# Kernel optimization log

Hardware: AMD Instinct MI355X
Metric: run time of the kernel (lower is better)

Reference implementation:

```python
import jax, jax.numpy as jnp
import numpy as np

B, T, E, H, D = 4, 2048, 1024, 16, 64  # batch, seq(block_size), n_embed, num_heads, hidden_dim


def setup_inputs() -> dict:
    key = jax.random.key(0)
    ks = jax.random.split(key, 10)
    s_in = 1.0 / np.sqrt(E)
    return {
        "x": jax.random.normal(ks[0], (B, T, E), dtype=jnp.float32),
        "Wq": jax.random.normal(ks[1], (H, E, D), dtype=jnp.float32) * s_in,
        "bq": jnp.zeros((H, D), dtype=jnp.float32),
        "Wk": jax.random.normal(ks[2], (H, E, D), dtype=jnp.float32) * s_in,
        "bk": jnp.zeros((H, D), dtype=jnp.float32),
        "Wv": jax.random.normal(ks[3], (H, E, D), dtype=jnp.float32) * s_in,
        "bv": jnp.zeros((H, D), dtype=jnp.float32),
        "Wp": jax.random.normal(ks[4], (E, E), dtype=jnp.float32) * s_in,
        "bp": jnp.zeros((E,), dtype=jnp.float32),
    }


def reference(x, Wq, bq, Wk, bk, Wv, bv, Wp, bp):
    # Batched equivalent of the per-head Python loop: each head h computes
    # causal scaled-dot-product attention with its own Q/K/V projections.
    q = jnp.einsum("bte,hed->bhtd", x, Wq) + bq[None, :, None, :]
    k = jnp.einsum("bte,hed->bhtd", x, Wk) + bk[None, :, None, :]
    v = jnp.einsum("bte,hed->bhtd", x, Wv) + bv[None, :, None, :]
    scale = 1.0 / jnp.sqrt(jnp.asarray(D, dtype=x.dtype))
    scores = jnp.einsum("bhtd,bhsd->bhts", q, k) * scale  # [B,H,T,T]
    causal = jnp.tril(jnp.ones((T, T), dtype=bool))
    scores = jnp.where(causal[None, None, :, :], scores, jnp.asarray(-jnp.inf, dtype=x.dtype))
    att = jax.nn.softmax(scores, axis=-1)
    head_out = jnp.einsum("bhts,bhsd->bhtd", att, v)  # [B,H,T,D]
    # concat heads along last dim: [B,T,H*D] == [B,T,E]
    cat = head_out.transpose(0, 2, 1, 3).reshape(B, T, H * D)
    out = cat @ Wp + bp  # final projection (dropout is identity in eval)
    return out
```

## Files before the change

kernel.cpp:

```cpp
#include <hip/hip_runtime.h>


typedef __attribute__((ext_vector_type(8))) __bf16 bf16x8;
typedef __attribute__((ext_vector_type(4))) float f32x4;
typedef __attribute__((ext_vector_type(16))) float f32x16;
typedef __attribute__((ext_vector_type(4))) unsigned int u32x4;
typedef __attribute__((ext_vector_type(2))) unsigned int u32x2;
typedef unsigned short u16;
typedef unsigned int u32;

#define DEV __device__ __forceinline__

#define QK_SCALE 0.18033688011112042f

DEV u16 f2bf(float f) {
  u32 u = __builtin_bit_cast(u32, f);
  u += 0x7fffu + ((u >> 16) & 1u);
  return (u16)(u >> 16);
}
DEV u32 pack2(float a, float b) { return (u32)f2bf(a) | ((u32)f2bf(b) << 16); }

DEV float exp2_hw(float x) { float r; asm("v_exp_f32 %0, %1" : "=v"(r) : "v"(x)); return r; }
DEV u32 cvtpk_bf16(float lo, float hi) {
  u32 r; asm("v_cvt_pk_bf16_f32 %0, %1, %2" : "=v"(r) : "v"(lo), "v"(hi)); return r;
}
DEV void pl32swap(u32& a, u32& b) { asm("v_permlane32_swap_b32 %0, %1" : "+v"(a), "+v"(b)); }
DEV float max3f(float a, float b, float c) {
  float r; asm("v_max3_f32 %0, %1, %2, %3" : "=v"(r) : "v"(a), "v"(b), "v"(c)); return r;
}

DEV f32x16 zero16() { f32x16 z;
#pragma unroll
  for (int i = 0; i < 16; i++) z[i] = 0.f;
  return z; }

DEV void gll16(const u16* g, u16* l) {
  __builtin_amdgcn_global_load_lds((const __attribute__((address_space(1))) void*)g,
                                   (__attribute__((address_space(3))) void*)l, 16, 0, 0);
}

#define SCHEDB() __builtin_amdgcn_sched_barrier(0)
#define SBAR()   do { __builtin_amdgcn_s_barrier(); SCHEDB(); } while (0)
#define LGKM0()  do { asm volatile("s_waitcnt lgkmcnt(0)" ::: "memory"); SCHEDB(); } while (0)

__global__ __launch_bounds__(256) void prep_x_kernel(
    const float* __restrict__ x, const float* __restrict__ bq, const float* __restrict__ bk,
    const float* __restrict__ bv, u16* __restrict__ xbf, float* __restrict__ bqkv) {
  int gid = blockIdx.x * 256 + threadIdx.x;
  if (gid < 3072) {
    float v = (gid < 1024) ? bq[gid] * QK_SCALE : (gid < 2048 ? bk[gid - 1024] : bv[gid - 2048]);
    bqkv[gid] = v;
  }
  const float4* xv = (const float4*)x;
  float4 f0 = xv[(size_t)gid * 2];
  float4 f1 = xv[(size_t)gid * 2 + 1];
  u32x4 st;
  st.x = pack2(f0.x, f0.y); st.y = pack2(f0.z, f0.w);
  st.z = pack2(f1.x, f1.y); st.w = pack2(f1.z, f1.w);
  *(u32x4*)&xbf[(size_t)gid * 8] = st;
}

__global__ __launch_bounds__(256) void prep_w_kernel(
    const float* __restrict__ Wq, const float* __restrict__ Wk, const float* __restrict__ Wv,
    const float* __restrict__ Wp, u16* __restrict__ wqkvT, u16* __restrict__ wpT) {
  __shared__ float t[64][65];
  int bid = blockIdx.x, tid = threadIdx.x;
  int r0 = tid >> 6, c = tid & 63;
  if (bid < 768) {
    int p = bid >> 8, rem = bid & 255, h = rem >> 4, et = rem & 15;
    float sc = (p == 0) ? QK_SCALE : 1.0f;
    const float* src = (p == 0 ? Wq : (p == 1 ? Wk : Wv)) + ((size_t)h * 1024 + et * 64) * 64;
#pragma unroll
    for (int i = 0; i < 16; i++) { int e = r0 + i * 4; t[e][c] = src[(size_t)e * 64 + c]; }
    __syncthreads();
    u16* dst = wqkvT + ((size_t)p * 1024 + h * 64) * 1024 + et * 64;
#pragma unroll
    for (int i = 0; i < 16; i++) { int d = r0 + i * 4; dst[(size_t)d * 1024 + c] = f2bf(t[c][d] * sc); }
  } else {
    int b2 = bid - 768, rt = b2 >> 4, ct = b2 & 15;
#pragma unroll
    for (int i = 0; i < 16; i++) { int e = r0 + i * 4; t[e][c] = Wp[(size_t)(rt * 64 + e) * 1024 + ct * 64 + c]; }
    __syncthreads();
#pragma unroll
    for (int i = 0; i < 16; i++) { int f = r0 + i * 4; wpT[(size_t)(ct * 64 + f) * 1024 + rt * 64 + c] = f2bf(t[c][f]); }
  }
}

#define SLOT_U16 24576

DEV void stageA_unit(const u16* __restrict__ Asrc, int row0, int k0, int h, u16* An, int tid) {
#pragma unroll
  for (int jj = 0; jj < 2; jj++) {
    int idx = jj * 512 + tid;
    int row = h * 128 + (idx >> 3), slot = idx & 7;
    int ss = slot ^ (row & 7);
    gll16(Asrc + (size_t)(row0 + row) * 1024 + k0 + ss * 8, An + (size_t)row * 64 + slot * 8);
  }
}
DEV void stageB_unit(const u16* __restrict__ Bsrc, int row0, int k0, int h, u16* Bn, int tid) {
  int idx = tid;
  int row = h * 64 + (idx >> 3), slot = idx & 7;
  int ss = slot ^ (row & 7);
  gll16(Bsrc + (size_t)(row0 + row) * 1024 + k0 + ss * 8, Bn + (size_t)row * 64 + slot * 8);
}

DEV bf16x8 ldsAB(const u16* base, int row, int kk, int lg) {
  return *(const bf16x8*)&base[row * 64 + (((lg + kk * 4) ^ (row & 7)) * 8)];
}

__global__ __launch_bounds__(512, 2) void gemm256_kernel(
    const u16* __restrict__ A, const u16* __restrict__ Bt, const float* __restrict__ bias,
    int tilesN, int mode, u16* __restrict__ Qb, u16* __restrict__ Kb, u16* __restrict__ VTb,
    float* __restrict__ outF) {
  __shared__ u16 lds[3 * SLOT_U16];
  int nwg = gridDim.x;
  int bid = blockIdx.x;
  int swz = (bid % 8) * (nwg / 8) + bid / 8;
  int bm = swz / tilesN, bn = swz % tilesN;
  int tid = threadIdx.x;
  int lane = tid & 63, wave = tid >> 6;
  int wm = wave >> 1, wn = wave & 1;
  int lr = lane & 15, lg = lane >> 4;
  int aRow0 = bm * 256, bRow0 = bn * 128;
  int ar = wm * 64, br = wn * 64;

  f32x4 acc[4][4];
#pragma unroll
  for (int i = 0; i < 4; i++)
#pragma unroll
    for (int j = 0; j < 4; j++) acc[i][j] = f32x4{0.f, 0.f, 0.f, 0.f};

#pragma unroll
  for (int pt = 0; pt < 2; pt++) {
    u16* As = lds + pt * SLOT_U16;
    stageA_unit(A, aRow0, pt * 64, 0, As, tid);
    stageA_unit(A, aRow0, pt * 64, 1, As, tid);
    stageB_unit(Bt, bRow0, pt * 64, 0, As + 16384, tid);
    stageB_unit(Bt, bRow0, pt * 64, 1, As + 16384, tid);
  }
  asm volatile("s_waitcnt vmcnt(6)" ::: "memory");
  SCHEDB();
  SBAR();

  int rs = 0;
  for (int t = 0; t < 16; ++t) {
    u16* Ac = lds + rs * SLOT_U16;
    u16* Bc = Ac + 16384;
    int ws = rs + 2; if (ws >= 3) ws -= 3;
    u16* An = lds + ws * SLOT_U16;
    u16* Bn = An + 16384;
    int k2 = (t + 2) * 64;
    bool st = (t + 2) < 16;

    bf16x8 aLo[2][2], bLo[2][2];
#pragma unroll
    for (int i = 0; i < 2; i++)
#pragma unroll
      for (int kk = 0; kk < 2; kk++) aLo[i][kk] = ldsAB(Ac, ar + i * 16 + lr, kk, lg);
#pragma unroll
    for (int j = 0; j < 2; j++)
#pragma unroll
      for (int kk = 0; kk < 2; kk++) bLo[j][kk] = ldsAB(Bc, br + j * 16 + lr, kk, lg);
    if (st) stageA_unit(A, aRow0, k2, 0, An, tid);
    SBAR(); LGKM0();
    __builtin_amdgcn_s_setprio(1);
#pragma unroll
    for (int kk = 0; kk < 2; kk++)
#pragma unroll
      for (int i = 0; i < 2; i++)
#pragma unroll
        for (int j = 0; j < 2; j++)
          acc[i][j] = __builtin_amdgcn_mfma_f32_16x16x32_bf16(aLo[i][kk], bLo[j][kk], acc[i][j], 0, 0, 0);
    __builtin_amdgcn_s_setprio(0);
    SBAR();

    bf16x8 bHi[2][2];
#pragma unroll
    for (int j = 0; j < 2; j++)
#pragma unroll
      for (int kk = 0; kk < 2; kk++) bHi[j][kk] = ldsAB(Bc, br + 32 + j * 16 + lr, kk, lg);
    if (st) stageB_unit(Bt, bRow0, k2, 0, Bn, tid);
    SBAR(); LGKM0();
    __builtin_amdgcn_s_setprio(1);
#pragma unroll
    for (int kk = 0; kk < 2; kk++)
#pragma unroll
      for (int i = 0; i < 2; i++)
#pragma unroll
        for (int j = 0; j < 2; j++)
          acc[i][j + 2] = __builtin_amdgcn_mfma_f32_16x16x32_bf16(aLo[i][kk], bHi[j][kk], acc[i][j + 2], 0, 0, 0);
    __builtin_amdgcn_s_setprio(0);
    SBAR();

    bf16x8 aHi[2][2];
#pragma unroll
    for (int i = 0; i < 2; i++)
#pragma unroll
      for (int kk = 0; kk < 2; kk++) aHi[i][kk] = ldsAB(Ac, ar + 32 + i * 16 + lr, kk, lg);
    if (st) stageA_unit(A, aRow0, k2, 1, An, tid);
    SBAR(); LGKM0();
    __builtin_amdgcn_s_setprio(1);
#pragma unroll
    for (int kk = 0; kk < 2; kk++)
#pragma unroll
      for (int i = 0; i < 2; i++)
#pragma unroll
        for (int j = 0; j < 2; j++)
          acc[i + 2][j + 2] = __builtin_amdgcn_mfma_f32_16x16x32_bf16(aHi[i][kk], bHi[j][kk], acc[i + 2][j + 2], 0, 0, 0);
    __builtin_amdgcn_s_setprio(0);
    SBAR();

    if (st) stageB_unit(Bt, bRow0, k2, 1, Bn, tid);
    SBAR();
    __builtin_amdgcn_s_setprio(1);
#pragma unroll
    for (int kk = 0; kk < 2; kk++)
#pragma unroll
      for (int i = 0; i < 2; i++)
#pragma unroll
        for (int j = 0; j < 2; j++)
          acc[i + 2][j] = __builtin_amdgcn_mfma_f32_16x16x32_bf16(aHi[i][kk], bLo[j][kk], acc[i + 2][j], 0, 0, 0);
    __builtin_amdgcn_s_setprio(0);
    if (t < 14) { asm volatile("s_waitcnt vmcnt(6)" ::: "memory"); }
    else if (t == 14) { asm volatile("s_waitcnt vmcnt(0)" ::: "memory"); }
    SCHEDB();
    SBAR();

    rs = (rs == 2) ? 0 : rs + 1;
  }

  int crow = aRow0 + wm * 64;
  int ccol = bRow0 + wn * 64;
  if (mode == 0) {
#pragma unroll
    for (int j = 0; j < 4; j++) {
      int col = ccol + j * 16 + lr;
      float bb = bias[col];
      int p = col >> 10, h = (col >> 6) & 15, d = col & 63;
#pragma unroll
      for (int i = 0; i < 4; i++) {
        int row0 = crow + i * 16 + lg * 4;
        int b_ = row0 >> 11, t0 = row0 & 2047;
        if (p == 2) {
          u32x2 pv;
          pv.x = pack2(acc[i][j][0] + bb, acc[i][j][1] + bb);
          pv.y = pack2(acc[i][j][2] + bb, acc[i][j][3] + bb);
          *(u32x2*)&VTb[((size_t)(b_ * 16 + h) * 64 + d) * 2048 + t0] = pv;
        } else {
          u16* dst = (p == 0 ? Qb : Kb);
#pragma unroll
          for (int r = 0; r < 4; r++)
            dst[((size_t)(b_ * 16 + h) * 2048 + (t0 + r)) * 64 + d] = f2bf(acc[i][j][r] + bb);
        }
      }
    }
  } else {
#pragma unroll
    for (int j = 0; j < 4; j++) {
      int col = ccol + j * 16 + lr;
      float bb = bias[col];
#pragma unroll
      for (int i = 0; i < 4; i++) {
        int row0 = crow + i * 16 + lg * 4;
#pragma unroll
        for (int r = 0; r < 4; r++)
          outF[(size_t)(row0 + r) * 1024 + col] = acc[i][j][r] + bb;
      }
    }
  }
}

DEV void stage_kv128(const u16* __restrict__ Kh, const u16* __restrict__ Vh, int kv0,
                     u16* Ksb, u16* Vsb, int tid) {
#pragma unroll
  for (int j = 0; j < 4; j++) {
    int ci = j * 128 + tid;
    int row = ci >> 3, slot = ci & 7;
    int ss = slot ^ (row & 7);
    __builtin_amdgcn_global_load_lds(
        (const __attribute__((address_space(1))) void*)(Kh + (size_t)(kv0 + row) * 64 + ss * 8),
        (__attribute__((address_space(3))) void*)(Ksb + ci * 8), 16, 0, 0);
    __builtin_amdgcn_global_load_lds(
        (const __attribute__((address_space(1))) void*)(Vh + (size_t)row * 2048 + kv0 + ss * 8),
        (__attribute__((address_space(3))) void*)(Vsb + ci * 8), 16, 0, 0);
  }
}

__global__ __launch_bounds__(128, 2) void attn_kernel(
    const u16* __restrict__ Qb, const u16* __restrict__ Kb, const u16* __restrict__ VTb,
    u16* __restrict__ cat) {
  __shared__ u16 Ks[2][64 * 64];
  __shared__ u16 Vs[2][64 * 64];
  int bid = blockIdx.x;
  int t = 31 - (bid >> 6);
  int bh = bid & 63;
  int b = bh >> 4, h = bh & 15;
  int tid = threadIdx.x, wave = tid >> 6, lane = tid & 63;
  int l31 = lane & 31, hi = lane >> 5;
  int qrow = t * 64 + wave * 32 + l31;

  const u16* Qh = Qb + (size_t)bh * 2048 * 64;
  const u16* Kh = Kb + (size_t)bh * 2048 * 64;
  const u16* Vh = VTb + (size_t)bh * 64 * 2048;

  bf16x8 qf[4];
#pragma unroll
  for (int ks = 0; ks < 4; ks++)
    qf[ks] = *(const bf16x8*)&Qh[(size_t)qrow * 64 + ks * 16 + hi * 8];

  u32 loff[4];
#pragma unroll
  for (int ks = 0; ks < 4; ks++)
    loff[ks] = (u32)(l31 * 128 + (((ks * 2 + hi) ^ (l31 & 7)) * 16));

  f32x16 o0 = zero16(), o1 = zero16();
  float m_run = -1e30f, l_run = 0.f;
  int iters = t + 1;

  stage_kv128(Kh, Vh, 0, Ks[0], Vs[0], tid);
  __syncthreads();
  int cur = 0;

  for (int kvt = 0; kvt < iters; ++kvt) {
    int kv0 = kvt * 64;
    if (kvt + 1 < iters) stage_kv128(Kh, Vh, kv0 + 64, Ks[cur ^ 1], Vs[cur ^ 1], tid);

    f32x16 s0 = zero16(), s1 = zero16();
    const char* kb = (const char*)&Ks[cur][0];
    __builtin_amdgcn_s_setprio(1);
#pragma unroll
    for (int ks = 0; ks < 4; ks++) {
      bf16x8 k0 = *(const bf16x8*)(kb + loff[ks]);
      bf16x8 k1 = *(const bf16x8*)(kb + loff[ks] + 4096);
      s0 = __builtin_amdgcn_mfma_f32_32x32x16_bf16(k0, qf[ks], s0, 0, 0, 0);
      s1 = __builtin_amdgcn_mfma_f32_32x32x16_bf16(k1, qf[ks], s1, 0, 0, 0);
    }
    __builtin_amdgcn_s_setprio(0);

    if (kvt == t) {
      int relh = qrow - kv0 - 4 * hi;
#pragma unroll
      for (int r = 0; r < 16; r++) {
        int off = (r & 3) + 8 * (r >> 2);
        s0[r] = (off > relh) ? -1e30f : s0[r];
        s1[r] = (off + 32 > relh) ? -1e30f : s1[r];
      }
    }

    float ta = max3f(s0[0], s0[1], s0[2]);
    float tb = max3f(s0[4], s0[5], s0[6]);
    float tc = max3f(s0[8], s0[9], s0[10]);
    float td = max3f(s0[12], s0[13], s0[14]);
    ta = max3f(ta, s0[3], s1[0]);
    tb = max3f(tb, s0[7], s1[4]);
    tc = max3f(tc, s0[11], s1[8]);
    td = max3f(td, s0[15], s1[12]);
    ta = max3f(ta, s1[1], s1[2]);
    tb = max3f(tb, s1[5], s1[6]);
    tc = max3f(tc, s1[9], s1[10]);
    td = max3f(td, s1[13], s1[14]);
    ta = max3f(ta, s1[3], tb);
    tc = max3f(tc, s1[7], td);
    float tmax = max3f(ta, tc, s1[11]);
    tmax = fmaxf(tmax, s1[15]);
    tmax = fmaxf(tmax, __shfl_xor(tmax, 32));
    float corr = 1.f;
    if (!__all(tmax <= m_run + 8.f)) {
      float m_new = fmaxf(m_run, tmax);
      corr = exp2_hw(m_run - m_new);
      o0 = o0 * corr;
      o1 = o1 * corr;
      m_run = m_new;
    }
    float t0 = 0.f, t1 = 0.f, t2 = 0.f, t3 = 0.f;
#pragma unroll
    for (int j = 0; j < 4; j++) {
      float p00 = exp2_hw(s0[j * 4 + 0] - m_run); s0[j * 4 + 0] = p00; t0 += p00;
      float p01 = exp2_hw(s0[j * 4 + 1] - m_run); s0[j * 4 + 1] = p01; t1 += p01;
      float p02 = exp2_hw(s0[j * 4 + 2] - m_run); s0[j * 4 + 2] = p02; t2 += p02;
      float p03 = exp2_hw(s0[j * 4 + 3] - m_run); s0[j * 4 + 3] = p03; t3 += p03;
      float p10 = exp2_hw(s1[j * 4 + 0] - m_run); s1[j * 4 + 0] = p10; t0 += p10;
      float p11 = exp2_hw(s1[j * 4 + 1] - m_run); s1[j * 4 + 1] = p11; t1 += p11;
      float p12 = exp2_hw(s1[j * 4 + 2] - m_run); s1[j * 4 + 2] = p12; t2 += p12;
      float p13 = exp2_hw(s1[j * 4 + 3] - m_run); s1[j * 4 + 3] = p13; t3 += p13;
    }
    float ts = (t0 + t1) + (t2 + t3);
    ts += __shfl_xor(ts, 32);
    l_run = l_run * corr + ts;

    const char* vb = (const char*)&Vs[cur][0];
    __builtin_amdgcn_s_setprio(1);
#pragma unroll
    for (int ks = 0; ks < 4; ks++) {
      const f32x16& sb = (ks < 2) ? s0 : s1;
      int g2 = (ks & 1) * 8;
      u32 a  = cvtpk_bf16(sb[g2 + 0], sb[g2 + 1]);
      u32 c  = cvtpk_bf16(sb[g2 + 2], sb[g2 + 3]);
      u32 bb = cvtpk_bf16(sb[g2 + 4], sb[g2 + 5]);
      u32 d  = cvtpk_bf16(sb[g2 + 6], sb[g2 + 7]);
      pl32swap(a, bb);
      pl32swap(c, d);
      u32x4 wv; wv.x = a; wv.y = c; wv.z = bb; wv.w = d;
      bf16x8 pf = __builtin_bit_cast(bf16x8, wv);
      bf16x8 v0 = *(const bf16x8*)(vb + loff[ks]);
      bf16x8 v1 = *(const bf16x8*)(vb + loff[ks] + 4096);
      o0 = __builtin_amdgcn_mfma_f32_32x32x16_bf16(v0, pf, o0, 0, 0, 0);
      o1 = __builtin_amdgcn_mfma_f32_32x32x16_bf16(v1, pf, o1, 0, 0, 0);
    }
    __builtin_amdgcn_s_setprio(0);

    __syncthreads();
    cur ^= 1;
  }

  float li = 1.0f / l_run;
#pragma unroll
  for (int m = 0; m < 8; m++) {
    int dbase = 2 * (m & 1) + 8 * (m >> 1) + 4 * hi;
    u32 w0 = cvtpk_bf16(o0[2 * m] * li, o0[2 * m + 1] * li);
    u32 w1 = cvtpk_bf16(o1[2 * m] * li, o1[2 * m + 1] * li);
    *(u32*)&cat[(size_t)(b * 2048 + qrow) * 1024 + h * 64 + dbase] = w0;
    *(u32*)&cat[(size_t)(b * 2048 + qrow) * 1024 + h * 64 + 32 + dbase] = w1;
  }
}

extern "C" void kernel_launch(void* const* d_in, const int* in_sizes, int n_in,
                              void* d_out, int out_size, void* d_ws, size_t ws_size,
                              hipStream_t stream) {
  const float* x  = (const float*)d_in[0];
  const float* Wq = (const float*)d_in[1];
  const float* bq = (const float*)d_in[2];
  const float* Wk = (const float*)d_in[3];
  const float* bk = (const float*)d_in[4];
  const float* Wv = (const float*)d_in[5];
  const float* bv = (const float*)d_in[6];
  const float* Wp = (const float*)d_in[7];
  const float* bp = (const float*)d_in[8];

  char* w = (char*)d_ws;
  u16* xbf    = (u16*)w;                 w += (size_t)8192 * 1024 * 2;
  u16* wqkvT  = (u16*)w;                 w += (size_t)3072 * 1024 * 2;
  u16* wpT    = (u16*)w;                 w += (size_t)1024 * 1024 * 2;
  float* bqkv = (float*)w;               w += (size_t)3072 * 4;
  u16* Qb     = (u16*)w;                 w += (size_t)64 * 2048 * 64 * 2;
  u16* Kb     = (u16*)w;                 w += (size_t)64 * 2048 * 64 * 2;
  u16* VTb    = (u16*)w;                 w += (size_t)64 * 64 * 2048 * 2;
  u16* cat    = (u16*)w;                 w += (size_t)8192 * 1024 * 2;

  prep_x_kernel<<<4096, 256, 0, stream>>>(x, bq, bk, bv, xbf, bqkv);
  prep_w_kernel<<<1024, 256, 0, stream>>>(Wq, Wk, Wv, Wp, wqkvT, wpT);
  gemm256_kernel<<<768, 512, 0, stream>>>(xbf, wqkvT, bqkv, 24, 0, Qb, Kb, VTb, nullptr);
  attn_kernel<<<2048, 128, 0, stream>>>(Qb, Kb, VTb, cat);
  gemm256_kernel<<<256, 512, 0, stream>>>(cat, wpT, bp, 8, 1, nullptr, nullptr, nullptr, (float*)d_out);
}
```

Before: 166.0 us.

## Restructure GEMM k-step from four MFMA phases into two with full A fragment

The GEMM main loop now loads all four A row fragments up front and splits each k-step into two compute phases of 16 MFMAs instead of four phases of 8. Global-to-LDS staging for both A halves and both B halves is issued together, which cuts the barriers per iteration roughly in half. An explicit lgkmcnt wait is placed before the first barrier. This raises register pressure from holding more fragments and reduces how finely the global loads are interleaved with compute, and the vmcnt accounting now runs against a different load-issue pattern.

```diff
diff --git a/kernel.cpp b/kernel.cpp
--- a/kernel.cpp
+++ b/kernel.cpp
@@ -152,25 +152,30 @@
     int k2 = (t + 2) * 64;
     bool st = (t + 2) < 16;
 
-    bf16x8 aLo[2][2], bLo[2][2];
-#pragma unroll
-    for (int i = 0; i < 2; i++)
-#pragma unroll
-      for (int kk = 0; kk < 2; kk++) aLo[i][kk] = ldsAB(Ac, ar + i * 16 + lr, kk, lg);
+    bf16x8 aF[4][2], bLo[2][2];
+#pragma unroll
+    for (int i = 0; i < 4; i++)
+#pragma unroll
+      for (int kk = 0; kk < 2; kk++) aF[i][kk] = ldsAB(Ac, ar + i * 16 + lr, kk, lg);
 #pragma unroll
     for (int j = 0; j < 2; j++)
 #pragma unroll
       for (int kk = 0; kk < 2; kk++) bLo[j][kk] = ldsAB(Bc, br + j * 16 + lr, kk, lg);
-    if (st) stageA_unit(A, aRow0, k2, 0, An, tid);
+    if (st) {
+      stageA_unit(A, aRow0, k2, 0, An, tid);
+      stageA_unit(A, aRow0, k2, 1, An, tid);
+    }
+    asm volatile("s_waitcnt lgkmcnt(8)" ::: "memory");
+    SCHEDB();
     SBAR(); LGKM0();
     __builtin_amdgcn_s_setprio(1);
 #pragma unroll
     for (int kk = 0; kk < 2; kk++)
 #pragma unroll
-      for (int i = 0; i < 2; i++)
+      for (int i = 0; i < 4; i++)
 #pragma unroll
         for (int j = 0; j < 2; j++)
-          acc[i][j] = __builtin_amdgcn_mfma_f32_16x16x32_bf16(aLo[i][kk], bLo[j][kk], acc[i][j], 0, 0, 0);
+          acc[i][j] = __builtin_amdgcn_mfma_f32_16x16x32_bf16(aF[i][kk], bLo[j][kk], acc[i][j], 0, 0, 0);
     __builtin_amdgcn_s_setprio(0);
     SBAR();
 
@@ -179,47 +184,19 @@
     for (int j = 0; j < 2; j++)
 #pragma unroll
       for (int kk = 0; kk < 2; kk++) bHi[j][kk] = ldsAB(Bc, br + 32 + j * 16 + lr, kk, lg);
-    if (st) stageB_unit(Bt, bRow0, k2, 0, Bn, tid);
+    if (st) {
+      stageB_unit(Bt, bRow0, k2, 0, Bn, tid);
+      stageB_unit(Bt, bRow0, k2, 1, Bn, tid);
+    }
     SBAR(); LGKM0();
     __builtin_amdgcn_s_setprio(1);
 #pragma unroll
     for (int kk = 0; kk < 2; kk++)
 #pragma unroll
-      for (int i = 0; i < 2; i++)
+      for (int i = 0; i < 4; i++)
 #pragma unroll
         for (int j = 0; j < 2; j++)
-          acc[i][j + 2] = __builtin_amdgcn_mfma_f32_16x16x32_bf16(aLo[i][kk], bHi[j][kk], acc[i][j + 2], 0, 0, 0);
-    __builtin_amdgcn_s_setprio(0);
-    SBAR();
-
-    bf16x8 aHi[2][2];
-#pragma unroll
-    for (int i = 0; i < 2; i++)
-#pragma unroll
-      for (int kk = 0; kk < 2; kk++) aHi[i][kk] = ldsAB(Ac, ar + 32 + i * 16 + lr, kk, lg);
-    if (st) stageA_unit(A, aRow0, k2, 1, An, tid);
-    SBAR(); LGKM0();
-    __builtin_amdgcn_s_setprio(1);
-#pragma unroll
-    for (int kk = 0; kk < 2; kk++)
-#pragma unroll
-      for (int i = 0; i < 2; i++)
-#pragma unroll
-        for (int j = 0; j < 2; j++)
-          acc[i + 2][j + 2] = __builtin_amdgcn_mfma_f32_16x16x32_bf16(aHi[i][kk], bHi[j][kk], acc[i + 2][j + 2], 0, 0, 0);
-    __builtin_amdgcn_s_setprio(0);
-    SBAR();
-
-    if (st) stageB_unit(Bt, bRow0, k2, 1, Bn, tid);
-    SBAR();
-    __builtin_amdgcn_s_setprio(1);
-#pragma unroll
-    for (int kk = 0; kk < 2; kk++)
-#pragma unroll
-      for (int i = 0; i < 2; i++)
-#pragma unroll
-        for (int j = 0; j < 2; j++)
-          acc[i + 2][j] = __builtin_amdgcn_mfma_f32_16x16x32_bf16(aHi[i][kk], bLo[j][kk], acc[i + 2][j], 0, 0, 0);
+          acc[i][j + 2] = __builtin_amdgcn_mfma_f32_16x16x32_bf16(aF[i][kk], bHi[j][kk], acc[i][j + 2], 0, 0, 0);
     __builtin_amdgcn_s_setprio(0);
     if (t < 14) { asm volatile("s_waitcnt vmcnt(6)" ::: "memory"); }
     else if (t == 14) { asm volatile("s_waitcnt vmcnt(0)" ::: "memory"); }
```

New measurement: 161.7 us. 1.03x faster.
